# Kernel tuning notes

Measured on AMD Instinct MI355X. Metric: run time of the kernel, lower is better.

Reference implementation:

```python
import jax, jax.numpy as jnp
import numpy as np


def setup_inputs() -> dict:
    key = jax.random.key(0)
    k1, k2, k3 = jax.random.split(key, 3)
    B, t_dim, h_dim = 32, 256, 512
    h, w, M = 64, 64, 128
    H = jax.random.normal(k1, (B, h_dim, h, w), dtype=jnp.float32)
    W = jax.random.normal(k2, (B, t_dim, M), dtype=jnp.float32)
    # 1x1 conv weight [h_dim, t_dim, 1, 1] collapses to a [h_dim, t_dim] matmul
    head_w = jax.random.normal(k3, (h_dim, t_dim), dtype=jnp.float32) * (t_dim ** -0.5)
    return {"H": H, "W": W, "head_w": head_w}


def reference(H, W, head_w):
    S = H.shape                                   # [B, h_dim, h, w]
    Hf = H.reshape(S[0], S[1], -1)                # [B, h_dim, N]
    Wp = jnp.einsum('ht,btm->bhm', head_w, W)     # 1x1 conv proj: [B, h_dim, M]
    scores = jnp.einsum('bhn,bhm->bnm', Hf, Wp)   # [B, N, M]
    A = jax.nn.softmax(scores, axis=2)            # softmax over words M
    C = jnp.einsum('bnm,bhm->bnh', A, Wp)         # [B, N, h_dim]
    C = jnp.transpose(C, (0, 2, 1))               # [B, h_dim, N]
    return C.reshape(S)
```

## Files before the change

### kernel.cpp

```cpp
#include <hip/hip_runtime.h>

#define BB 32
#define TD 256
#define HD 512
#define MM 128
#define NN 4096

typedef __attribute__((ext_vector_type(8))) short short8;
typedef __attribute__((ext_vector_type(4))) float floatx4;

__device__ inline unsigned int bf16_rne(float f) {
    unsigned int u = __float_as_uint(f);
    return (u + 0x7fffu + ((u >> 16) & 1u)) >> 16;
}
__device__ inline float quad16_max(float v) {
    v = fmaxf(v, __shfl_xor(v, 1));
    v = fmaxf(v, __shfl_xor(v, 2));
    v = fmaxf(v, __shfl_xor(v, 4));
    v = fmaxf(v, __shfl_xor(v, 8));
    return v;
}
__device__ inline float quad16_sum(float v) {
    v += __shfl_xor(v, 1);
    v += __shfl_xor(v, 2);
    v += __shfl_xor(v, 4);
    v += __shfl_xor(v, 8);
    return v;
}

__device__ __forceinline__ void gload16(const void* gptr, void* ldsptr) {
    __builtin_amdgcn_global_load_lds(
        (const __attribute__((address_space(1))) void*)gptr,
        (__attribute__((address_space(3))) void*)ldsptr,
        16, 0, 0);
}

__global__ __launch_bounds__(256, 2) void wp_kernel(
    const float* __restrict__ Wmat,
    const float* __restrict__ head_w,
    unsigned short* __restrict__ Wpt_hi,
    unsigned short* __restrict__ Wpt_lo,
    unsigned short* __restrict__ Wp_b)
{
    const int tid = threadIdx.x;
    const int tx = tid & 31;
    const int ty = tid >> 5;
    const int b  = blockIdx.y;
    const int h0 = blockIdx.x * 64;

    __shared__ float s_hw[64][64];
    __shared__ float s_w[64][128];

    float acc[8][4];
#pragma unroll
    for (int r = 0; r < 8; ++r)
#pragma unroll
        for (int c = 0; c < 4; ++c) acc[r][c] = 0.f;

    for (int t0 = 0; t0 < TD; t0 += 64) {
#pragma unroll
        for (int k = 0; k < 4; ++k) {
            int i = (tid >> 4) + 16 * k;
            int j = (tid & 15) * 4;
            *(float4*)&s_hw[i][j] = *(const float4*)&head_w[(h0 + i) * TD + t0 + j];
        }
#pragma unroll
        for (int k = 0; k < 8; ++k) {
            int i = (tid >> 5) + 8 * k;
            *(float4*)&s_w[i][(tid & 31) * 4] =
                *(const float4*)&Wmat[((b * TD) + t0 + i) * MM + (tid & 31) * 4];
        }
        __syncthreads();
#pragma unroll 4
        for (int tt = 0; tt < 64; ++tt) {
            float b4[4];
            *(float4*)b4 = *(const float4*)&s_w[tt][tx * 4];
#pragma unroll
            for (int r = 0; r < 8; ++r) {
                float a = s_hw[ty * 8 + r][tt];
#pragma unroll
                for (int c = 0; c < 4; ++c) acc[r][c] += a * b4[c];
            }
        }
        __syncthreads();
    }

#pragma unroll
    for (int r = 0; r < 8; ++r) {
        unsigned int p0 = bf16_rne(acc[r][0]) | (bf16_rne(acc[r][1]) << 16);
        unsigned int p1 = bf16_rne(acc[r][2]) | (bf16_rne(acc[r][3]) << 16);
        uint2 v; v.x = p0; v.y = p1;
        *(uint2*)&Wp_b[((size_t)(b * HD) + h0 + ty * 8 + r) * MM + tx * 4] = v;
    }
#pragma unroll
    for (int c = 0; c < 4; ++c) {
        unsigned int hw4[4], lw4[4];
#pragma unroll
        for (int rp = 0; rp < 4; ++rp) {
            float x0 = acc[2 * rp][c], x1 = acc[2 * rp + 1][c];
            unsigned int u0 = __float_as_uint(x0), u1 = __float_as_uint(x1);
            float l0 = x0 - __uint_as_float(u0 & 0xffff0000u);
            float l1 = x1 - __uint_as_float(u1 & 0xffff0000u);
            hw4[rp] = (u0 >> 16) | (u1 & 0xffff0000u);
            lw4[rp] = bf16_rne(l0) | (bf16_rne(l1) << 16);
        }
        size_t base = ((size_t)(b * MM) + tx * 4 + c) * HD + h0 + ty * 8;
        *(uint4*)&Wpt_hi[base] = make_uint4(hw4[0], hw4[1], hw4[2], hw4[3]);
        *(uint4*)&Wpt_lo[base] = make_uint4(lw4[0], lw4[1], lw4[2], lw4[3]);
    }
}

__global__ __launch_bounds__(256, 2) void fused_kernel(
    const float* __restrict__ H,
    const unsigned short* __restrict__ Wpt_hi,
    const unsigned short* __restrict__ Wpt_lo,
    const unsigned short* __restrict__ Wp_b,
    float* __restrict__ out)
{
    __shared__ __align__(16) unsigned char smem[65536];
    const int tid = threadIdx.x;
    const int w   = tid >> 6;
    const int L   = tid & 63;
    const int q   = L >> 4;
    const int l15 = L & 15;
    const int b   = blockIdx.y;
    const int n0  = blockIdx.x * 128;

    const int nh = (w & 1) * 64;
    const int mh = (w >> 1) * 64;

    const float* Hb = H + ((size_t)b * HD) * NN + n0;
    const unsigned short* WptH = Wpt_hi + (size_t)b * MM * HD;
    const unsigned short* WptL = Wpt_lo + (size_t)b * MM * HD;

    floatx4 acc[4][4];
#pragma unroll
    for (int nt = 0; nt < 4; ++nt)
#pragma unroll
        for (int mt = 0; mt < 4; ++mt) acc[nt][mt] = (floatx4){0.f, 0.f, 0.f, 0.f};

    const int sa_n = (w & 1) * 64 + L;
    const int sa_h = (w >> 1) * 16;
    const int u0   = (w >> 1) * 2;

    int aw_off[2];
#pragma unroll
    for (int ii = 0; ii < 2; ++ii)
        aw_off[ii] = sa_n * 64 + (((u0 + ii) ^ (sa_n & 3)) * 16);

    int bg_off[2];
#pragma unroll
    for (int k = 0; k < 2; ++k) {
        int flat = tid + 256 * k;
        int m = flat >> 2, uu = flat & 3;
        bg_off[k] = m * HD + ((uu ^ (m & 3)) * 8);
    }
    const int wave_lds = (tid & 192) * 16;

    float xa[16];
    const float* srcA = Hb + (size_t)sa_h * NN + sa_n;

#pragma unroll
    for (int k = 0; k < 2; ++k) {
        gload16(WptH + bg_off[k], smem + 32768 + wave_lds + 256 * 16 * k);
        gload16(WptL + bg_off[k], smem + 49152 + wave_lds + 256 * 16 * k);
    }
#pragma unroll
    for (int t = 0; t < 16; ++t) xa[t] = srcA[(size_t)t * NN];

#pragma unroll 1
    for (int c = 0; c < 16; ++c) {
        const int p = c & 1;
        unsigned char* AhP = smem + p * 8192;
        unsigned char* AlP = smem + 16384 + p * 8192;

#pragma unroll
        for (int ii = 0; ii < 2; ++ii) {
            unsigned int hp[4], lp[4];
#pragma unroll
            for (int jp = 0; jp < 4; ++jp) {
                float x0 = xa[ii * 8 + 2 * jp], x1 = xa[ii * 8 + 2 * jp + 1];
                unsigned int v0 = __float_as_uint(x0), v1 = __float_as_uint(x1);
                float l0 = x0 - __uint_as_float(v0 & 0xffff0000u);
                float l1 = x1 - __uint_as_float(v1 & 0xffff0000u);
                hp[jp] = (v0 >> 16) | (v1 & 0xffff0000u);
                lp[jp] = bf16_rne(l0) | (bf16_rne(l1) << 16);
            }
            *(uint4*)(AhP + aw_off[ii]) = make_uint4(hp[0], hp[1], hp[2], hp[3]);
            *(uint4*)(AlP + aw_off[ii]) = make_uint4(lp[0], lp[1], lp[2], lp[3]);
        }
        asm volatile("s_waitcnt vmcnt(0) lgkmcnt(0)" ::: "memory");
        __builtin_amdgcn_s_barrier();
        __builtin_amdgcn_sched_barrier(0);

        if (c + 1 < 16) {
            const int h0n = 32 * (c + 1);
            unsigned char* BhN = smem + 32768 + (p ^ 1) * 8192;
            unsigned char* BlN = smem + 49152 + (p ^ 1) * 8192;
#pragma unroll
            for (int k = 0; k < 2; ++k) {
                gload16(WptH + h0n + bg_off[k], BhN + wave_lds + 256 * 16 * k);
                gload16(WptL + h0n + bg_off[k], BlN + wave_lds + 256 * 16 * k);
            }
            srcA += (size_t)32 * NN;
#pragma unroll
            for (int t = 0; t < 16; ++t) xa[t] = srcA[(size_t)t * NN];
        }

        const unsigned char* BhP = smem + 32768 + p * 8192;
        const unsigned char* BlP = smem + 49152 + p * 8192;
        short8 ahf[4], alf[4], bhf[4], blf[4];
#pragma unroll
        for (int nt = 0; nt < 4; ++nt) {
            int n = nh + nt * 16 + l15;
            int off = n * 64 + ((q ^ (n & 3)) * 16);
            ahf[nt] = *(const short8*)(AhP + off);
            alf[nt] = *(const short8*)(AlP + off);
        }
#pragma unroll
        for (int mt = 0; mt < 4; ++mt) {
            int m = mh + mt * 16 + l15;
            int off = m * 64 + ((q ^ (m & 3)) * 16);
            bhf[mt] = *(const short8*)(BhP + off);
            blf[mt] = *(const short8*)(BlP + off);
        }
        __builtin_amdgcn_s_setprio(1);
#pragma unroll
        for (int nt = 0; nt < 4; ++nt)
#pragma unroll
            for (int mt = 0; mt < 4; ++mt) {
                acc[nt][mt] = __builtin_amdgcn_mfma_f32_16x16x32_bf16(ahf[nt], bhf[mt], acc[nt][mt], 0, 0, 0);
                acc[nt][mt] = __builtin_amdgcn_mfma_f32_16x16x32_bf16(alf[nt], bhf[mt], acc[nt][mt], 0, 0, 0);
                acc[nt][mt] = __builtin_amdgcn_mfma_f32_16x16x32_bf16(ahf[nt], blf[mt], acc[nt][mt], 0, 0, 0);
            }
        __builtin_amdgcn_s_setprio(0);
    }

    float* redmax = (float*)(smem + 32768);
    float* redsum = (float*)(smem + 32768 + 1024);
    const int mhalf = w >> 1;

    float rmax[4][4];
#pragma unroll
    for (int nt = 0; nt < 4; ++nt)
#pragma unroll
        for (int r = 0; r < 4; ++r) {
            float v = fmaxf(fmaxf(acc[nt][0][r], acc[nt][1][r]),
                            fmaxf(acc[nt][2][r], acc[nt][3][r]));
            rmax[nt][r] = quad16_max(v);
        }
    if (l15 == 0) {
#pragma unroll
        for (int nt = 0; nt < 4; ++nt)
#pragma unroll
            for (int r = 0; r < 4; ++r)
                redmax[mhalf * 128 + nh + nt * 16 + q * 4 + r] = rmax[nt][r];
    }
    __syncthreads();
    float gmax[4][4], rsum[4][4];
#pragma unroll
    for (int nt = 0; nt < 4; ++nt)
#pragma unroll
        for (int r = 0; r < 4; ++r) {
            gmax[nt][r] = fmaxf(rmax[nt][r],
                                redmax[(1 - mhalf) * 128 + nh + nt * 16 + q * 4 + r]);
            float s = 0.f;
#pragma unroll
            for (int mt = 0; mt < 4; ++mt) {
                float e = __expf(acc[nt][mt][r] - gmax[nt][r]);
                acc[nt][mt][r] = e;
                s += e;
            }
            rsum[nt][r] = quad16_sum(s);
        }
    if (l15 == 0) {
#pragma unroll
        for (int nt = 0; nt < 4; ++nt)
#pragma unroll
            for (int r = 0; r < 4; ++r)
                redsum[mhalf * 128 + nh + nt * 16 + q * 4 + r] = rsum[nt][r];
    }
    __syncthreads();

    unsigned char* As = smem;
#pragma unroll
    for (int nt = 0; nt < 4; ++nt)
#pragma unroll
        for (int r = 0; r < 4; ++r) {
            int n = nh + nt * 16 + q * 4 + r;
            float inv = 1.f / (rsum[nt][r] + redsum[(1 - mhalf) * 128 + n]);
#pragma unroll
            for (int mt = 0; mt < 4; ++mt) {
                int m = mh + mt * 16 + l15;
                unsigned short v = (unsigned short)bf16_rne(acc[nt][mt][r] * inv);
                *(unsigned short*)(As + n * 256 + (((m >> 3) ^ (n & 15)) * 16) + (m & 7) * 2) = v;
            }
        }
    __syncthreads();

    const int hq = (w >> 1) * 32;
    const unsigned short* WpB = Wp_b + (size_t)b * HD * MM;
    float* outb = out + ((size_t)b * HD) * NN + n0;

    int wg_off[4];
#pragma unroll
    for (int k = 0; k < 4; ++k) {
        int flat = tid + 256 * k;
        int hrow = flat >> 4, uu = flat & 15;
        wg_off[k] = hrow * MM + ((uu ^ (hrow & 15)) * 8);
    }
#pragma unroll
    for (int k = 0; k < 4; ++k)
        gload16(WpB + wg_off[k], smem + 32768 + wave_lds + 256 * 16 * k);

    short8 af[4][4];
#pragma unroll
    for (int nt = 0; nt < 4; ++nt)
#pragma unroll
        for (int ks = 0; ks < 4; ++ks) {
            int n = nh + nt * 16 + l15;
            af[nt][ks] = *(short8*)(As + n * 256 + (((q + 4 * ks) ^ (n & 15)) * 16));
        }

#pragma unroll 1
    for (int hc = 0; hc < 8; ++hc) {
        const int p = hc & 1;
        if (hc == 0) { asm volatile("s_waitcnt vmcnt(0)" ::: "memory"); }
        else         { asm volatile("s_waitcnt vmcnt(8)" ::: "memory"); }
        __builtin_amdgcn_sched_barrier(0);
        __builtin_amdgcn_s_barrier();
        __builtin_amdgcn_sched_barrier(0);
        if (hc + 1 < 8) {
            const unsigned short* Wsrc = WpB + (size_t)(hc + 1) * 64 * MM;
            unsigned char* WbN = smem + 32768 + (p ^ 1) * 16384;
#pragma unroll
            for (int k = 0; k < 4; ++k)
                gload16(Wsrc + wg_off[k], WbN + wave_lds + 256 * 16 * k);
        }

        const unsigned char* WbP = smem + 32768 + p * 16384;
        floatx4 accB[4][2];
#pragma unroll
        for (int nt = 0; nt < 4; ++nt)
#pragma unroll
            for (int ht = 0; ht < 2; ++ht) accB[nt][ht] = (floatx4){0.f, 0.f, 0.f, 0.f};

#pragma unroll
        for (int ks = 0; ks < 4; ++ks) {
            short8 bf[2];
#pragma unroll
            for (int ht = 0; ht < 2; ++ht) {
                int hl = hq + ht * 16 + l15;
                bf[ht] = *(const short8*)(WbP + hl * 256 + (((q + 4 * ks) ^ (hl & 15)) * 16));
            }
#pragma unroll
            for (int nt = 0; nt < 4; ++nt)
#pragma unroll
                for (int ht = 0; ht < 2; ++ht)
                    accB[nt][ht] = __builtin_amdgcn_mfma_f32_16x16x32_bf16(af[nt][ks], bf[ht], accB[nt][ht], 0, 0, 0);
        }
#pragma unroll
        for (int nt = 0; nt < 4; ++nt)
#pragma unroll
            for (int ht = 0; ht < 2; ++ht) {
                int hglob = hc * 64 + hq + ht * 16 + l15;
                int nrow = nh + nt * 16 + q * 4;
                *(floatx4*)(outb + (size_t)hglob * NN + nrow) = accB[nt][ht];
            }
    }
}

extern "C" void kernel_launch(void* const* d_in, const int* in_sizes, int n_in,
                              void* d_out, int out_size, void* d_ws, size_t ws_size,
                              hipStream_t stream)
{
    (void)in_sizes; (void)n_in; (void)out_size; (void)ws_size;
    const float* H      = (const float*)d_in[0];
    const float* Wmat   = (const float*)d_in[1];
    const float* head_w = (const float*)d_in[2];
    float* out = (float*)d_out;

    unsigned short* Wpt_hi = (unsigned short*)d_ws;
    unsigned short* Wpt_lo = Wpt_hi + (size_t)BB * MM * HD;
    unsigned short* Wp_b   = Wpt_lo + (size_t)BB * MM * HD;

    wp_kernel<<<dim3(HD / 64, BB), 256, 0, stream>>>(Wmat, head_w, Wpt_hi, Wpt_lo, Wp_b);
    fused_kernel<<<dim3(NN / 128, BB), 256, 0, stream>>>(H, Wpt_hi, Wpt_lo, Wp_b, out);
}
```

Baseline: 489.6 us.

## Software-pipeline phase-1 score loop with double-buffered H register prefetch

```diff
diff --git a/kernel.cpp b/kernel.cpp
--- a/kernel.cpp
+++ b/kernel.cpp
@@ -157,84 +157,117 @@
     }
     const int wave_lds = (tid & 192) * 16;
 
-    float xa[16];
-    const float* srcA = Hb + (size_t)sa_h * NN + sa_n;
-
+    float xaA[16], xaB[16];
+    const float* srcNext = Hb + (size_t)sa_h * NN + sa_n;
+
+#define P1_CONV(PDST, SRC)                                                    \
+    do {                                                                      \
+        unsigned char* AhN_ = smem + (PDST) * 8192;                           \
+        unsigned char* AlN_ = smem + 16384 + (PDST) * 8192;                   \
+        _Pragma("unroll")                                                     \
+        for (int ii = 0; ii < 2; ++ii) {                                      \
+            unsigned int hp_[4], lp_[4];                                      \
+            _Pragma("unroll")                                                 \
+            for (int jp = 0; jp < 4; ++jp) {                                  \
+                float x0 = SRC[ii * 8 + 2 * jp], x1 = SRC[ii * 8 + 2 * jp + 1];\
+                unsigned int v0 = __float_as_uint(x0), v1 = __float_as_uint(x1);\
+                float l0 = x0 - __uint_as_float(v0 & 0xffff0000u);            \
+                float l1 = x1 - __uint_as_float(v1 & 0xffff0000u);            \
+                hp_[jp] = (v0 >> 16) | (v1 & 0xffff0000u);                    \
+                lp_[jp] = bf16_rne(l0) | (bf16_rne(l1) << 16);                \
+            }                                                                 \
+            *(uint4*)(AhN_ + aw_off[ii]) = make_uint4(hp_[0], hp_[1], hp_[2], hp_[3]);\
+            *(uint4*)(AlN_ + aw_off[ii]) = make_uint4(lp_[0], lp_[1], lp_[2], lp_[3]);\
+        }                                                                     \
+    } while (0)
+
+#define P1_MFMA(PP)                                                           \
+    do {                                                                      \
+        const unsigned char* AhP_ = smem + (PP) * 8192;                       \
+        const unsigned char* AlP_ = smem + 16384 + (PP) * 8192;               \
+        const unsigned char* BhP_ = smem + 32768 + (PP) * 8192;               \
+        const unsigned char* BlP_ = smem + 49152 + (PP) * 8192;               \
+        short8 ahf_[4], alf_[4], bhf_[4], blf_[4];                            \
+        _Pragma("unroll")                                                     \
+        for (int nt = 0; nt < 4; ++nt) {                                      \
+            int n_ = nh + nt * 16 + l15;                                      \
+            int off_ = n_ * 64 + ((q ^ (n_ & 3)) * 16);                       \
+            ahf_[nt] = *(const short8*)(AhP_ + off_);                         \
+            alf_[nt] = *(const short8*)(AlP_ + off_);                         \
+        }                                                                     \
+        _Pragma("unroll")                                                     \
+        for (int mt = 0; mt < 4; ++mt) {                                      \
+            int m_ = mh + mt * 16 + l15;                                      \
+            int off_ = m_ * 64 + ((q ^ (m_ & 3)) * 16);                       \
+            bhf_[mt] = *(const short8*)(BhP_ + off_);                         \
+            blf_[mt] = *(const short8*)(BlP_ + off_);                         \
+        }                                                                     \
+        __builtin_amdgcn_s_setprio(1);                                        \
+        _Pragma("unroll")                                                     \
+        for (int nt = 0; nt < 4; ++nt)                                        \
+            _Pragma("unroll")                                                 \
+            for (int mt = 0; mt < 4; ++mt) {                                  \
+                acc[nt][mt] = __builtin_amdgcn_mfma_f32_16x16x32_bf16(ahf_[nt], bhf_[mt], acc[nt][mt], 0, 0, 0);\
+                acc[nt][mt] = __builtin_amdgcn_mfma_f32_16x16x32_bf16(alf_[nt], bhf_[mt], acc[nt][mt], 0, 0, 0);\
+                acc[nt][mt] = __builtin_amdgcn_mfma_f32_16x16x32_bf16(ahf_[nt], blf_[mt], acc[nt][mt], 0, 0, 0);\
+            }                                                                 \
+        __builtin_amdgcn_s_setprio(0);                                        \
+    } while (0)
+
+#define P1_ITER(J, CUR, NXT, LOADXA)                                          \
+    do {                                                                      \
+        asm volatile("s_waitcnt vmcnt(16) lgkmcnt(0)" ::: "memory");          \
+        __builtin_amdgcn_s_barrier();                                         \
+        __builtin_amdgcn_sched_barrier(0);                                    \
+        const int p_ = (J) & 1;                                               \
+        {                                  \
+            const int h0n_ = 32 * ((J) + 1);                                  \
+            unsigned char* BhN_ = smem + 32768 + (p_ ^ 1) * 8192;             \
+            unsigned char* BlN_ = smem + 49152 + (p_ ^ 1) * 8192;             \
+            _Pragma("unroll")                                                 \
+            for (int k = 0; k < 2; ++k) {                                     \
+                gload16(WptH + h0n_ + bg_off[k], BhN_ + wave_lds + 4096 * k); \
+                gload16(WptL + h0n_ + bg_off[k], BlN_ + wave_lds + 4096 * k); \
+            }                                                                 \
+        }                                                                     \
+        if (LOADXA) {                                      \
+            _Pragma("unroll")                                                 \
+            for (int t = 0; t < 16; ++t) NXT[t] = srcNext[(size_t)t * NN];    \
+            srcNext += (size_t)32 * NN;                                       \
+        }                                                                     \
+        __builtin_amdgcn_sched_barrier(0);                                    \
+        P1_MFMA(p_);                                                          \
+        P1_CONV(p_ ^ 1, CUR);                  \
+    } while (0)
+
+#pragma unroll
+    for (int t = 0; t < 16; ++t) xaB[t] = srcNext[(size_t)t * NN];
+    srcNext += (size_t)32 * NN;
 #pragma unroll
     for (int k = 0; k < 2; ++k) {
-        gload16(WptH + bg_off[k], smem + 32768 + wave_lds + 256 * 16 * k);
-        gload16(WptL + bg_off[k], smem + 49152 + wave_lds + 256 * 16 * k);
-    }
-#pragma unroll
-    for (int t = 0; t < 16; ++t) xa[t] = srcA[(size_t)t * NN];
+        gload16(WptH + bg_off[k], smem + 32768 + wave_lds + 4096 * k);
+        gload16(WptL + bg_off[k], smem + 49152 + wave_lds + 4096 * k);
+    }
+#pragma unroll
+    for (int t = 0; t < 16; ++t) xaA[t] = srcNext[(size_t)t * NN];
+    srcNext += (size_t)32 * NN;
+    P1_CONV(0, xaB);
 
 #pragma unroll 1
-    for (int c = 0; c < 16; ++c) {
-        const int p = c & 1;
-        unsigned char* AhP = smem + p * 8192;
-        unsigned char* AlP = smem + 16384 + p * 8192;
-
-#pragma unroll
-        for (int ii = 0; ii < 2; ++ii) {
-            unsigned int hp[4], lp[4];
-#pragma unroll
-            for (int jp = 0; jp < 4; ++jp) {
-                float x0 = xa[ii * 8 + 2 * jp], x1 = xa[ii * 8 + 2 * jp + 1];
-                unsigned int v0 = __float_as_uint(x0), v1 = __float_as_uint(x1);
-                float l0 = x0 - __uint_as_float(v0 & 0xffff0000u);
-                float l1 = x1 - __uint_as_float(v1 & 0xffff0000u);
-                hp[jp] = (v0 >> 16) | (v1 & 0xffff0000u);
-                lp[jp] = bf16_rne(l0) | (bf16_rne(l1) << 16);
-            }
-            *(uint4*)(AhP + aw_off[ii]) = make_uint4(hp[0], hp[1], hp[2], hp[3]);
-            *(uint4*)(AlP + aw_off[ii]) = make_uint4(lp[0], lp[1], lp[2], lp[3]);
-        }
-        asm volatile("s_waitcnt vmcnt(0) lgkmcnt(0)" ::: "memory");
-        __builtin_amdgcn_s_barrier();
-        __builtin_amdgcn_sched_barrier(0);
-
-        if (c + 1 < 16) {
-            const int h0n = 32 * (c + 1);
-            unsigned char* BhN = smem + 32768 + (p ^ 1) * 8192;
-            unsigned char* BlN = smem + 49152 + (p ^ 1) * 8192;
-#pragma unroll
-            for (int k = 0; k < 2; ++k) {
-                gload16(WptH + h0n + bg_off[k], BhN + wave_lds + 256 * 16 * k);
-                gload16(WptL + h0n + bg_off[k], BlN + wave_lds + 256 * 16 * k);
-            }
-            srcA += (size_t)32 * NN;
-#pragma unroll
-            for (int t = 0; t < 16; ++t) xa[t] = srcA[(size_t)t * NN];
-        }
-
-        const unsigned char* BhP = smem + 32768 + p * 8192;
-        const unsigned char* BlP = smem + 49152 + p * 8192;
-        short8 ahf[4], alf[4], bhf[4], blf[4];
-#pragma unroll
-        for (int nt = 0; nt < 4; ++nt) {
-            int n = nh + nt * 16 + l15;
-            int off = n * 64 + ((q ^ (n & 3)) * 16);
-            ahf[nt] = *(const short8*)(AhP + off);
-            alf[nt] = *(const short8*)(AlP + off);
-        }
-#pragma unroll
-        for (int mt = 0; mt < 4; ++mt) {
-            int m = mh + mt * 16 + l15;
-            int off = m * 64 + ((q ^ (m & 3)) * 16);
-            bhf[mt] = *(const short8*)(BhP + off);
-            blf[mt] = *(const short8*)(BlP + off);
-        }
-        __builtin_amdgcn_s_setprio(1);
-#pragma unroll
-        for (int nt = 0; nt < 4; ++nt)
-#pragma unroll
-            for (int mt = 0; mt < 4; ++mt) {
-                acc[nt][mt] = __builtin_amdgcn_mfma_f32_16x16x32_bf16(ahf[nt], bhf[mt], acc[nt][mt], 0, 0, 0);
-                acc[nt][mt] = __builtin_amdgcn_mfma_f32_16x16x32_bf16(alf[nt], bhf[mt], acc[nt][mt], 0, 0, 0);
-                acc[nt][mt] = __builtin_amdgcn_mfma_f32_16x16x32_bf16(ahf[nt], blf[mt], acc[nt][mt], 0, 0, 0);
-            }
-        __builtin_amdgcn_s_setprio(0);
-    }
+    for (int jj = 0; jj < 14; jj += 2) {
+        P1_ITER(jj, xaA, xaB, 1);
+        P1_ITER(jj + 1, xaB, xaA, 1);
+    }
+    P1_ITER(14, xaA, xaB, 0);
+
+    asm volatile("s_waitcnt vmcnt(0) lgkmcnt(0)" ::: "memory");
+    __builtin_amdgcn_s_barrier();
+    __builtin_amdgcn_sched_barrier(0);
+    P1_MFMA(1);
+
+#undef P1_ITER
+#undef P1_MFMA
+#undef P1_CONV
 
     float* redmax = (float*)(smem + 32768);
     float* redsum = (float*)(smem + 32768 + 1024);
```

New measurement: 490.3 us. About the same (+0.2%).
